# Performance work log

Measured on AMD Instinct MI355X. Metric: run time of the kernel, lower is better.

Reference implementation:

```python
import jax, jax.numpy as jnp
import numpy as np

N1, C, T1, V = 16, 64, 512, 25
NH, DK, DV, BD = 8, 64, 64, 64
DKH, DVH = DK // NH, DV // NH
NB = T1 // BD


def rel_to_abs(x):
    # x: (..., L, 2L-1) -> (..., L, L)  (rel-shift trick)
    *lead, L, _ = x.shape
    x = jnp.pad(x, [(0, 0)] * (x.ndim - 1) + [(0, 1)])      # (..., L, 2L)
    x = x.reshape(*lead, L * 2 * L)
    x = jnp.pad(x, [(0, 0)] * (x.ndim - 1) + [(0, L - 1)])
    x = x.reshape(*lead, L + 1, 2 * L - 1)
    return x[..., :L, L - 1:]


def setup_inputs() -> dict:
    key = jax.random.key(0)
    ks = jax.random.split(key, 6)
    return {
        "x": jax.random.normal(ks[0], (N1, C, T1, V), jnp.float32),
        "w_qkv": jax.random.normal(ks[1], (2 * DK + DV, C), jnp.float32) * 0.05,
        "b_qkv": jax.random.normal(ks[2], (2 * DK + DV,), jnp.float32) * 0.01,
        "w_out": jax.random.normal(ks[3], (DV, DV), jnp.float32) * 0.05,
        "b_out": jax.random.normal(ks[4], (DV,), jnp.float32) * 0.01,
        "key_rel": jax.random.normal(ks[5], (2 * BD - 1, DKH), jnp.float32),
    }


def reference(x, w_qkv, b_qkv, w_out, b_out, key_rel):
    B = N1 * V
    # (N1,C,T1,V) -> (N1*V, C, T1); 1x1 qkv conv == GEMM over channels
    xr = x.transpose(0, 3, 1, 2).reshape(B, C, T1)
    qkv = jnp.einsum('oc,bct->bot', w_qkv, xr) + b_qkv[None, :, None]
    q, k, v = qkv[:, :DK], qkv[:, DK:2 * DK], qkv[:, 2 * DK:]
    # split heads and blocks: (B, NH, dh, NB, BD); all blocks vectorized
    q = q.reshape(B, NH, DKH, NB, BD) * (DKH ** -0.5)
    k = k.reshape(B, NH, DKH, NB, BD)
    v = v.reshape(B, NH, DVH, NB, BD)
    logits = jnp.einsum('bhdnt,bhdns->bhnts', q, k)          # (B,NH,NB,BD,BD)
    # relative position logits (rel-shift)
    qb = q.transpose(0, 1, 3, 4, 2)                          # (B,NH,NB,BD,DKH)
    rel = jnp.einsum('bhntd,md->bhntm', qb, key_rel)         # (B,NH,NB,BD,2BD-1)
    logits = logits + rel_to_abs(rel)
    weights = jax.nn.softmax(logits, axis=-1)
    out = jnp.einsum('bhnts,bhdns->bhdnt', weights, v)       # (B,NH,DVH,NB,BD)
    # combine heads (head-major channels) and blocks along T
    out = out.reshape(B, DV, T1)
    ao = jnp.einsum('oc,bct->bot', w_out, out) + b_out[None, :, None]
    ao = ao.reshape(N1, V, DV, T1).transpose(0, 2, 3, 1)     # (N1,DV,T1,V)
    return jax.nn.relu(ao + x)
```

## Files before the change

kernel.cpp:

```cpp
#include <hip/hip_runtime.h>
#include <math.h>

#define Vc 25
#define QSCALE 0.5100697243f

#if __has_builtin(__builtin_amdgcn_mfma_f32_16x16x16bf16_1k)
#define HAVE_MFMA16 1
#define MFMA16(a, b, c) __builtin_amdgcn_mfma_f32_16x16x16bf16_1k(a, b, c, 0, 0, 0)
#else
#define HAVE_MFMA16 0
#endif

typedef short bf16x8 __attribute__((ext_vector_type(8), may_alias));
typedef short bf16x4 __attribute__((ext_vector_type(4), may_alias));
typedef unsigned int u32x2a __attribute__((ext_vector_type(2), may_alias));
typedef float f32x4 __attribute__((ext_vector_type(4)));

#define FENCE() asm volatile("" ::: "memory")

__device__ __forceinline__ unsigned short f2bf(float f) {
    unsigned u = __builtin_bit_cast(unsigned, f);
    u = (u + 0x7fff + ((u >> 16) & 1)) >> 16;
    return (unsigned short)u;
}
__device__ __forceinline__ unsigned short f2bf_fast(float f) {
    unsigned u = __builtin_bit_cast(unsigned, f) + 0x8000u;
    return (unsigned short)(u >> 16);
}
__device__ __forceinline__ unsigned pkbf(float lo, float hi) {
    unsigned a = __builtin_bit_cast(unsigned, lo) + 0x8000u;
    unsigned b = __builtin_bit_cast(unsigned, hi) + 0x8000u;
    return __builtin_amdgcn_perm(b, a, 0x07060302);
}
__device__ __forceinline__ float bf2f(unsigned short h) {
    unsigned u = ((unsigned)h) << 16;
    return __builtin_bit_cast(float, u);
}

template<int CTRL>
__device__ __forceinline__ float dpp_add(float x) {
    int xi = __builtin_bit_cast(int, x);
    int yi = __builtin_amdgcn_update_dpp(0, xi, CTRL, 0xf, 0xf, true);
    return x + __builtin_bit_cast(float, yi);
}
__device__ __forceinline__ float row_sum16(float s) {
    s = dpp_add<0xB1>(s);
    s = dpp_add<0x4E>(s);
    s = dpp_add<0x141>(s);
    s = dpp_add<0x140>(s);
    return s;
}

#define WQA_O 0
#define BQ_O  12288
#define KRT_O 12672
#define WOA_O 13760

__global__ void prep_kernel(const float* __restrict__ w_qkv, const float* __restrict__ b_qkv,
                            const float* __restrict__ w_out, const float* __restrict__ key_rel,
                            unsigned short* __restrict__ ws)
{
    const int gid = blockIdx.x * 256 + threadIdx.x;
    const int gsz = gridDim.x * 256;
    for (int id = gid; id < 12288; id += gsz) {
        int j = id & 7, lane = (id >> 3) & 63, ks = (id >> 9) & 1, mt = id >> 10;
        int m = mt * 16 + (lane & 15);
        int k = ks * 32 + (lane >> 4) * 8 + j;
        ws[WQA_O + id] = f2bf(w_qkv[m * 64 + k] * (m < 64 ? QSCALE : 1.f));
    }
    float* bq = (float*)(ws + BQ_O);
    for (int id = gid; id < 192; id += gsz)
        bq[id] = b_qkv[id] * (id < 64 ? QSCALE : 1.f);
    for (int id = gid; id < 1088; id += gsz) {
        int d = id & 7, m = id >> 3;
        ws[KRT_O + id] = (m < 127) ? f2bf(key_rel[m * 8 + d]) : (unsigned short)0;
    }
    for (int id = gid; id < 4096; id += gsz) {
        int j = id & 7, lane = (id >> 3) & 63, mtg = id >> 9;
        int m = (mtg & 3) * 16 + (lane & 15);
        int k = (mtg >> 2) * 32 + (lane >> 4) * 8 + j;
        ws[WOA_O + id] = f2bf(w_out[m * 64 + k]);
    }
}

#define QT_O   0
#define KT_O   4096
#define VS_O   8192
#define OT_O   12800
#define SCR_O  15360
#define SMEM_U16 19968

__global__ __launch_bounds__(256, 4)
void tcn_attn(const float* __restrict__ x, const float* __restrict__ b_out,
              const unsigned short* __restrict__ ws, float* __restrict__ y)
{
    __shared__ unsigned short sm[SMEM_U16];

    const int tid  = threadIdx.x;
    const int lane = tid & 63;
    const int w    = tid >> 6;
    const int li   = lane & 15;
    const int lq   = lane >> 4;
    const int koff = lq * 8;
    const int koff4 = lq * 4;
    const int n    = blockIdx.x;
    const int b    = blockIdx.y;
    const int n1   = b / Vc;
    const int v    = b - n1 * Vc;
    const int t0   = n * 64;
    const int trow = 16 * w + li;
    const unsigned scr = SCR_O + w * 1152;

    const bf16x8 z8 = {0,0,0,0,0,0,0,0};
    const bf16x4 z4h = {0,0,0,0};
    const f32x4  z4 = {0.f,0.f,0.f,0.f};
    (void)z4h; (void)koff4;

    for (int i = tid; i < 1920; i += 256)
        *(bf16x8*)(sm + i * 8) = z8;

    float xres[16];
    f32x4 pacc[4];
    #pragma unroll
    for (int mt = 0; mt < 4; ++mt)
        #pragma unroll
        for (int r = 0; r < 4; ++r) {
            int o = mt * 16 + lq * 4 + r;
            xres[mt * 4 + r] = x[((n1 * 64 + o) * 512 + t0 + 16 * w + li) * Vc + v];
            pacc[mt][r] = b_out[o];
        }

    #pragma unroll
    for (int mt = 0; mt < 4; ++mt)
        #pragma unroll
        for (int r = 0; r < 4; ++r)
            sm[SCR_O + (16 * w + li) * 72 + mt * 16 + 4 * lq + r] = f2bf_fast(xres[mt * 4 + r]);
    __syncthreads();

    const unsigned short* wq = ws + WQA_O;
    const float* bq = (const float*)(ws + BQ_O);
    #pragma unroll
    for (int sec = 0; sec < 3; ++sec) {
        const int mt = sec * 4 + w;
        bf16x8 a0 = *(const bf16x8*)(wq + ((mt * 2 + 0) * 64 + lane) * 8);
        bf16x8 a1 = *(const bf16x8*)(wq + ((mt * 2 + 1) * 64 + lane) * 8);
        f32x4 acc[4];
        __builtin_amdgcn_s_setprio(1);
        #pragma unroll
        for (int nt = 0; nt < 4; ++nt) {
            #pragma unroll
            for (int r = 0; r < 4; ++r) acc[nt][r] = bq[mt * 16 + lq * 4 + r];
            bf16x8 b0 = *(const bf16x8*)(sm + SCR_O + (16 * nt + li) * 72 + koff);
            bf16x8 b1 = *(const bf16x8*)(sm + SCR_O + (16 * nt + li) * 72 + 32 + koff);
            acc[nt] = __builtin_amdgcn_mfma_f32_16x16x32_bf16(a0, b0, acc[nt], 0, 0, 0);
            acc[nt] = __builtin_amdgcn_mfma_f32_16x16x32_bf16(a1, b1, acc[nt], 0, 0, 0);
        }
        __builtin_amdgcn_s_setprio(0);
        const int h2 = 2 * w + (lq >> 1);
        if (sec < 2) {
            const unsigned base = (sec == 0 ? QT_O : KT_O) + h2 * 512 + (lq & 1) * 4;
            #pragma unroll
            for (int nt = 0; nt < 4; ++nt) {
                u32x2a p;
                p.x = pkbf(acc[nt][0], acc[nt][1]);
                p.y = pkbf(acc[nt][2], acc[nt][3]);
                *(u32x2a*)(sm + base + (16 * nt + li) * 8) = p;
            }
        } else {
            #pragma unroll
            for (int nt = 0; nt < 4; ++nt)
                #pragma unroll
                for (int r = 0; r < 4; ++r)
                    sm[VS_O + h2 * 576 + ((lq & 1) * 4 + r) * 72 + 16 * nt + li] = f2bf_fast(acc[nt][r]);
        }
    }
    __syncthreads();

    int bidx[4];
    bool ghi[4];
    #pragma unroll
    for (int r = 0; r < 4; ++r) {
        int d = li - 4 * lq - r + 15;
        bidx[r] = ((lane & 48) | (d & 15)) << 2;
        ghi[r]  = d >= 16;
    }

#if HAVE_MFMA16
    bf16x4 br4[5];
    #pragma unroll
    for (int j = 0; j < 5; ++j)
        br4[j] = *(const bf16x4*)(ws + KRT_O + (16 * (3 - w + j) + li) * 8 + koff4);

    auto FRONT = [&](int h, f32x4* qk, f32x4* rl) {
        bf16x4 aq = *(const bf16x4*)(sm + QT_O + h * 512 + trow * 8 + koff4);
        if (lane >= 32) aq = z4h;
        __builtin_amdgcn_s_setprio(1);
        #pragma unroll
        for (int nt = 0; nt < 4; ++nt) {
            bf16x4 bk = *(const bf16x4*)(sm + KT_O + h * 512 + (16 * nt + li) * 8 + koff4);
            qk[nt] = MFMA16(aq, bk, z4);
        }
        #pragma unroll
        for (int j = 0; j < 5; ++j)
            rl[j] = MFMA16(aq, br4[j], z4);
        __builtin_amdgcn_s_setprio(0);
    };
#else
    bf16x8 br[5];
    #pragma unroll
    for (int j = 0; j < 5; ++j)
        br[j] = *(const bf16x8*)(ws + KRT_O + (16 * (3 - w + j) + li) * 8 + koff);

    auto FRONT = [&](int h, f32x4* qk, f32x4* rl) {
        bf16x8 aq = *(const bf16x8*)(sm + QT_O + h * 512 + trow * 8 + koff);
        if (lane >= 16) aq = z8;
        __builtin_amdgcn_s_setprio(1);
        #pragma unroll
        for (int nt = 0; nt < 4; ++nt) {
            bf16x8 bk = *(const bf16x8*)(sm + KT_O + h * 512 + (16 * nt + li) * 8 + koff);
            qk[nt] = __builtin_amdgcn_mfma_f32_16x16x32_bf16(aq, bk, z4, 0, 0, 0);
        }
        #pragma unroll
        for (int j = 0; j < 5; ++j)
            rl[j] = __builtin_amdgcn_mfma_f32_16x16x32_bf16(aq, br[j], z4, 0, 0, 0);
        __builtin_amdgcn_s_setprio(0);
    };
#endif

    auto BPERM = [&](const f32x4* rl, float (*sr)[5]) {
        #pragma unroll
        for (int r = 0; r < 4; ++r)
            #pragma unroll
            for (int j = 0; j < 5; ++j)
                sr[r][j] = __builtin_bit_cast(float,
                        __builtin_amdgcn_ds_bpermute(bidx[r], __builtin_bit_cast(int, rl[j][r])));
    };

    f32x4 qk[4];
    float sr[4][5];
    {
        f32x4 rl0[5];
        FRONT(0, qk, rl0);
        BPERM(rl0, sr);
    }

    #pragma unroll
    for (int h = 0; h < 8; ++h) {
        f32x4 qkn[4], rln[5];
        if (h < 7) FRONT(h + 1, qkn, rln);
        bf16x8 ao[4];
        if ((h & 3) == 3) {
            const int g = h >> 2;
            #pragma unroll
            for (int mt = 0; mt < 4; ++mt)
                ao[mt] = *(const bf16x8*)(ws + WOA_O + ((g * 4 + mt) * 64 + lane) * 8);
        }
        float lsum[4] = {0.f, 0.f, 0.f, 0.f};
        #pragma unroll
        for (int r = 0; r < 4; ++r)
            #pragma unroll
            for (int nt = 0; nt < 4; ++nt) {
                float rv = ghi[r] ? sr[r][nt + 1] : sr[r][nt];
                float e = __builtin_amdgcn_exp2f(qk[nt][r] + rv);
                sm[scr + (4 * lq + r) * 72 + 16 * nt + li] = f2bf_fast(e);
                lsum[r] += e;
            }
        float linv[4];
        #pragma unroll
        for (int r = 0; r < 4; ++r)
            linv[r] = 1.0f / row_sum16(lsum[r]);
        FENCE();
        f32x4 av = z4;
        __builtin_amdgcn_s_setprio(1);
        #pragma unroll
        for (int ks = 0; ks < 2; ++ks) {
            bf16x8 aa = *(const bf16x8*)(sm + scr + li * 72 + ks * 32 + koff);
            bf16x8 bv = *(const bf16x8*)(sm + VS_O + h * 576 + (li & 7) * 72 + ks * 32 + koff);
            av = __builtin_amdgcn_mfma_f32_16x16x32_bf16(aa, bv, av, 0, 0, 0);
        }
        __builtin_amdgcn_s_setprio(0);
        float srn[4][5];
        if (h < 7) BPERM(rln, srn);
        if (li < 8) {
            #pragma unroll
            for (int r = 0; r < 4; ++r)
                sm[OT_O + (16 * w + 4 * lq + r) * 40 + (h & 3) * 8 + li] = f2bf_fast(av[r] * linv[r]);
        }
        if ((h & 3) == 3) {
            FENCE();
            bf16x8 bo = *(const bf16x8*)(sm + OT_O + trow * 40 + koff);
            __builtin_amdgcn_s_setprio(1);
            #pragma unroll
            for (int mt = 0; mt < 4; ++mt)
                pacc[mt] = __builtin_amdgcn_mfma_f32_16x16x32_bf16(ao[mt], bo, pacc[mt], 0, 0, 0);
            __builtin_amdgcn_s_setprio(0);
        }
        FENCE();
        if (h < 7) {
            #pragma unroll
            for (int i = 0; i < 4; ++i) qk[i] = qkn[i];
            #pragma unroll
            for (int r = 0; r < 4; ++r)
                #pragma unroll
                for (int j = 0; j < 5; ++j)
                    sr[r][j] = srn[r][j];
        }
    }

    #pragma unroll
    for (int mt = 0; mt < 4; ++mt)
        #pragma unroll
        for (int r = 0; r < 4; ++r) {
            int o = mt * 16 + lq * 4 + r;
            int idx = ((n1 * 64 + o) * 512 + t0 + 16 * w + li) * Vc + v;
            y[idx] = fmaxf(pacc[mt][r] + xres[mt * 4 + r], 0.f);
        }
}

extern "C" void kernel_launch(void* const* d_in, const int* in_sizes, int n_in,
                              void* d_out, int out_size, void* d_ws, size_t ws_size,
                              hipStream_t stream) {
    const float* x       = (const float*)d_in[0];
    const float* w_qkv   = (const float*)d_in[1];
    const float* b_qkv   = (const float*)d_in[2];
    const float* w_out   = (const float*)d_in[3];
    const float* b_out   = (const float*)d_in[4];
    const float* key_rel = (const float*)d_in[5];
    float* y = (float*)d_out;
    unsigned short* ws = (unsigned short*)d_ws;

    prep_kernel<<<dim3(96), dim3(256), 0, stream>>>(w_qkv, b_qkv, w_out, key_rel, ws);
    dim3 grid(512 / 64, 400);
    tcn_attn<<<grid, dim3(256), 0, stream>>>(x, b_out, ws, y);
}
```

Baseline: 203.5 us.

## Process two adjacent V columns per block with paired 8-byte global loads/stores

Each block now handles two neighbouring v indices (the last group handles one). x is read and y written as float2 pairs, and the whole attention pipeline runs twice per block. The aim is to halve the strided 4-byte global transactions over the innermost V dimension, which waste sector bandwidth, and to halve the grid size. In exchange each block does serial work for two columns, register pressure rises from holding two residual arrays, and the block count drops to 1664.

```diff
diff --git a/kernel.cpp b/kernel.cpp
--- a/kernel.cpp
+++ b/kernel.cpp
@@ -15,6 +15,7 @@
 typedef short bf16x4 __attribute__((ext_vector_type(4), may_alias));
 typedef unsigned int u32x2a __attribute__((ext_vector_type(2), may_alias));
 typedef float f32x4 __attribute__((ext_vector_type(4)));
+typedef float f32x2a __attribute__((ext_vector_type(2), aligned(4), may_alias));
 
 #define FENCE() asm volatile("" ::: "memory")
 
@@ -105,8 +106,10 @@
     const int koff4 = lq * 4;
     const int n    = blockIdx.x;
     const int b    = blockIdx.y;
-    const int n1   = b / Vc;
-    const int v    = b - n1 * Vc;
+    const int n1   = b / 13;
+    const int vg   = b - n1 * 13;
+    const int v0   = vg * 2;
+    const int nv   = (vg < 12) ? 2 : 1;
     const int t0   = n * 64;
     const int trow = 16 * w + li;
     const unsigned scr = SCR_O + w * 1152;
@@ -119,62 +122,27 @@
     for (int i = tid; i < 1920; i += 256)
         *(bf16x8*)(sm + i * 8) = z8;
 
-    float xres[16];
-    f32x4 pacc[4];
-    #pragma unroll
-    for (int mt = 0; mt < 4; ++mt)
-        #pragma unroll
-        for (int r = 0; r < 4; ++r) {
-            int o = mt * 16 + lq * 4 + r;
-            xres[mt * 4 + r] = x[((n1 * 64 + o) * 512 + t0 + 16 * w + li) * Vc + v];
-            pacc[mt][r] = b_out[o];
-        }
-
-    #pragma unroll
-    for (int mt = 0; mt < 4; ++mt)
-        #pragma unroll
-        for (int r = 0; r < 4; ++r)
-            sm[SCR_O + (16 * w + li) * 72 + mt * 16 + 4 * lq + r] = f2bf_fast(xres[mt * 4 + r]);
-    __syncthreads();
-
-    const unsigned short* wq = ws + WQA_O;
-    const float* bq = (const float*)(ws + BQ_O);
-    #pragma unroll
-    for (int sec = 0; sec < 3; ++sec) {
-        const int mt = sec * 4 + w;
-        bf16x8 a0 = *(const bf16x8*)(wq + ((mt * 2 + 0) * 64 + lane) * 8);
-        bf16x8 a1 = *(const bf16x8*)(wq + ((mt * 2 + 1) * 64 + lane) * 8);
-        f32x4 acc[4];
-        __builtin_amdgcn_s_setprio(1);
-        #pragma unroll
-        for (int nt = 0; nt < 4; ++nt) {
-            #pragma unroll
-            for (int r = 0; r < 4; ++r) acc[nt][r] = bq[mt * 16 + lq * 4 + r];
-            bf16x8 b0 = *(const bf16x8*)(sm + SCR_O + (16 * nt + li) * 72 + koff);
-            bf16x8 b1 = *(const bf16x8*)(sm + SCR_O + (16 * nt + li) * 72 + 32 + koff);
-            acc[nt] = __builtin_amdgcn_mfma_f32_16x16x32_bf16(a0, b0, acc[nt], 0, 0, 0);
-            acc[nt] = __builtin_amdgcn_mfma_f32_16x16x32_bf16(a1, b1, acc[nt], 0, 0, 0);
-        }
-        __builtin_amdgcn_s_setprio(0);
-        const int h2 = 2 * w + (lq >> 1);
-        if (sec < 2) {
-            const unsigned base = (sec == 0 ? QT_O : KT_O) + h2 * 512 + (lq & 1) * 4;
-            #pragma unroll
-            for (int nt = 0; nt < 4; ++nt) {
-                u32x2a p;
-                p.x = pkbf(acc[nt][0], acc[nt][1]);
-                p.y = pkbf(acc[nt][2], acc[nt][3]);
-                *(u32x2a*)(sm + base + (16 * nt + li) * 8) = p;
-            }
-        } else {
-            #pragma unroll
-            for (int nt = 0; nt < 4; ++nt)
-                #pragma unroll
-                for (int r = 0; r < 4; ++r)
-                    sm[VS_O + h2 * 576 + ((lq & 1) * 4 + r) * 72 + 16 * nt + li] = f2bf_fast(acc[nt][r]);
-        }
-    }
-    __syncthreads();
+    float xr0[16], xr1[16];
+    if (nv == 2) {
+        #pragma unroll
+        for (int mt = 0; mt < 4; ++mt)
+            #pragma unroll
+            for (int r = 0; r < 4; ++r) {
+                int o = mt * 16 + lq * 4 + r;
+                f32x2a p = *(const f32x2a*)&x[((n1 * 64 + o) * 512 + t0 + trow) * Vc + v0];
+                xr0[mt * 4 + r] = p.x;
+                xr1[mt * 4 + r] = p.y;
+            }
+    } else {
+        #pragma unroll
+        for (int mt = 0; mt < 4; ++mt)
+            #pragma unroll
+            for (int r = 0; r < 4; ++r) {
+                int o = mt * 16 + lq * 4 + r;
+                xr0[mt * 4 + r] = x[((n1 * 64 + o) * 512 + t0 + trow) * Vc + v0];
+                xr1[mt * 4 + r] = 0.f;
+            }
+    }
 
     int bidx[4];
     bool ghi[4];
@@ -184,6 +152,9 @@
         bidx[r] = ((lane & 48) | (d & 15)) << 2;
         ghi[r]  = d >= 16;
     }
+
+    const unsigned short* wq = ws + WQA_O;
+    const float* bq = (const float*)(ws + BQ_O);
 
 #if HAVE_MFMA16
     bf16x4 br4[5];
@@ -236,85 +207,157 @@
                         __builtin_amdgcn_ds_bpermute(bidx[r], __builtin_bit_cast(int, rl[j][r])));
     };
 
-    f32x4 qk[4];
-    float sr[4][5];
-    {
-        f32x4 rl0[5];
-        FRONT(0, qk, rl0);
-        BPERM(rl0, sr);
-    }
-
-    #pragma unroll
-    for (int h = 0; h < 8; ++h) {
-        f32x4 qkn[4], rln[5];
-        if (h < 7) FRONT(h + 1, qkn, rln);
-        bf16x8 ao[4];
-        if ((h & 3) == 3) {
-            const int g = h >> 2;
-            #pragma unroll
-            for (int mt = 0; mt < 4; ++mt)
-                ao[mt] = *(const bf16x8*)(ws + WOA_O + ((g * 4 + mt) * 64 + lane) * 8);
-        }
-        float lsum[4] = {0.f, 0.f, 0.f, 0.f};
-        #pragma unroll
-        for (int r = 0; r < 4; ++r)
+    auto DOV = [&](const float (&xr)[16], float (&yout)[16]) {
+        #pragma unroll
+        for (int mt = 0; mt < 4; ++mt)
+            #pragma unroll
+            for (int r = 0; r < 4; ++r)
+                sm[SCR_O + trow * 72 + mt * 16 + 4 * lq + r] = f2bf_fast(xr[mt * 4 + r]);
+        __syncthreads();
+
+        #pragma unroll
+        for (int sec = 0; sec < 3; ++sec) {
+            const int mt = sec * 4 + w;
+            bf16x8 a0 = *(const bf16x8*)(wq + ((mt * 2 + 0) * 64 + lane) * 8);
+            bf16x8 a1 = *(const bf16x8*)(wq + ((mt * 2 + 1) * 64 + lane) * 8);
+            f32x4 acc[4];
+            __builtin_amdgcn_s_setprio(1);
             #pragma unroll
             for (int nt = 0; nt < 4; ++nt) {
-                float rv = ghi[r] ? sr[r][nt + 1] : sr[r][nt];
-                float e = __builtin_amdgcn_exp2f(qk[nt][r] + rv);
-                sm[scr + (4 * lq + r) * 72 + 16 * nt + li] = f2bf_fast(e);
-                lsum[r] += e;
-            }
-        float linv[4];
-        #pragma unroll
-        for (int r = 0; r < 4; ++r)
-            linv[r] = 1.0f / row_sum16(lsum[r]);
-        FENCE();
-        f32x4 av = z4;
-        __builtin_amdgcn_s_setprio(1);
-        #pragma unroll
-        for (int ks = 0; ks < 2; ++ks) {
-            bf16x8 aa = *(const bf16x8*)(sm + scr + li * 72 + ks * 32 + koff);
-            bf16x8 bv = *(const bf16x8*)(sm + VS_O + h * 576 + (li & 7) * 72 + ks * 32 + koff);
-            av = __builtin_amdgcn_mfma_f32_16x16x32_bf16(aa, bv, av, 0, 0, 0);
-        }
-        __builtin_amdgcn_s_setprio(0);
-        float srn[4][5];
-        if (h < 7) BPERM(rln, srn);
-        if (li < 8) {
-            #pragma unroll
-            for (int r = 0; r < 4; ++r)
-                sm[OT_O + (16 * w + 4 * lq + r) * 40 + (h & 3) * 8 + li] = f2bf_fast(av[r] * linv[r]);
-        }
-        if ((h & 3) == 3) {
+                #pragma unroll
+                for (int r = 0; r < 4; ++r) acc[nt][r] = bq[mt * 16 + lq * 4 + r];
+                bf16x8 b0 = *(const bf16x8*)(sm + SCR_O + (16 * nt + li) * 72 + koff);
+                bf16x8 b1 = *(const bf16x8*)(sm + SCR_O + (16 * nt + li) * 72 + 32 + koff);
+                acc[nt] = __builtin_amdgcn_mfma_f32_16x16x32_bf16(a0, b0, acc[nt], 0, 0, 0);
+                acc[nt] = __builtin_amdgcn_mfma_f32_16x16x32_bf16(a1, b1, acc[nt], 0, 0, 0);
+            }
+            __builtin_amdgcn_s_setprio(0);
+            const int h2 = 2 * w + (lq >> 1);
+            if (sec < 2) {
+                const unsigned base = (sec == 0 ? QT_O : KT_O) + h2 * 512 + (lq & 1) * 4;
+                #pragma unroll
+                for (int nt = 0; nt < 4; ++nt) {
+                    u32x2a p;
+                    p.x = pkbf(acc[nt][0], acc[nt][1]);
+                    p.y = pkbf(acc[nt][2], acc[nt][3]);
+                    *(u32x2a*)(sm + base + (16 * nt + li) * 8) = p;
+                }
+            } else {
+                #pragma unroll
+                for (int nt = 0; nt < 4; ++nt)
+                    #pragma unroll
+                    for (int r = 0; r < 4; ++r)
+                        sm[VS_O + h2 * 576 + ((lq & 1) * 4 + r) * 72 + 16 * nt + li] = f2bf_fast(acc[nt][r]);
+            }
+        }
+        __syncthreads();
+
+        f32x4 pacc[4];
+        #pragma unroll
+        for (int mt = 0; mt < 4; ++mt)
+            #pragma unroll
+            for (int r = 0; r < 4; ++r)
+                pacc[mt][r] = b_out[mt * 16 + lq * 4 + r];
+
+        f32x4 qk[4];
+        float sr[4][5];
+        {
+            f32x4 rl0[5];
+            FRONT(0, qk, rl0);
+            BPERM(rl0, sr);
+        }
+
+        #pragma unroll
+        for (int h = 0; h < 8; ++h) {
+            f32x4 qkn[4], rln[5];
+            if (h < 7) FRONT(h + 1, qkn, rln);
+            bf16x8 ao[4];
+            if ((h & 3) == 3) {
+                const int g = h >> 2;
+                #pragma unroll
+                for (int mt = 0; mt < 4; ++mt)
+                    ao[mt] = *(const bf16x8*)(ws + WOA_O + ((g * 4 + mt) * 64 + lane) * 8);
+            }
+            float lsum[4] = {0.f, 0.f, 0.f, 0.f};
+            #pragma unroll
+            for (int r = 0; r < 4; ++r)
+                #pragma unroll
+                for (int nt = 0; nt < 4; ++nt) {
+                    float rv = ghi[r] ? sr[r][nt + 1] : sr[r][nt];
+                    float e = __builtin_amdgcn_exp2f(qk[nt][r] + rv);
+                    sm[scr + (4 * lq + r) * 72 + 16 * nt + li] = f2bf_fast(e);
+                    lsum[r] += e;
+                }
+            float linv[4];
+            #pragma unroll
+            for (int r = 0; r < 4; ++r)
+                linv[r] = 1.0f / row_sum16(lsum[r]);
             FENCE();
-            bf16x8 bo = *(const bf16x8*)(sm + OT_O + trow * 40 + koff);
+            f32x4 av = z4;
             __builtin_amdgcn_s_setprio(1);
             #pragma unroll
-            for (int mt = 0; mt < 4; ++mt)
-                pacc[mt] = __builtin_amdgcn_mfma_f32_16x16x32_bf16(ao[mt], bo, pacc[mt], 0, 0, 0);
+            for (int ks = 0; ks < 2; ++ks) {
+                bf16x8 aa = *(const bf16x8*)(sm + scr + li * 72 + ks * 32 + koff);
+                bf16x8 bv = *(const bf16x8*)(sm + VS_O + h * 576 + (li & 7) * 72 + ks * 32 + koff);
+                av = __builtin_amdgcn_mfma_f32_16x16x32_bf16(aa, bv, av, 0, 0, 0);
+            }
             __builtin_amdgcn_s_setprio(0);
-        }
-        FENCE();
-        if (h < 7) {
-            #pragma unroll
-            for (int i = 0; i < 4; ++i) qk[i] = qkn[i];
-            #pragma unroll
-            for (int r = 0; r < 4; ++r)
-                #pragma unroll
-                for (int j = 0; j < 5; ++j)
-                    sr[r][j] = srn[r][j];
-        }
-    }
-
-    #pragma unroll
-    for (int mt = 0; mt < 4; ++mt)
-        #pragma unroll
-        for (int r = 0; r < 4; ++r) {
-            int o = mt * 16 + lq * 4 + r;
-            int idx = ((n1 * 64 + o) * 512 + t0 + 16 * w + li) * Vc + v;
-            y[idx] = fmaxf(pacc[mt][r] + xres[mt * 4 + r], 0.f);
-        }
+            float srn[4][5];
+            if (h < 7) BPERM(rln, srn);
+            if (li < 8) {
+                #pragma unroll
+                for (int r = 0; r < 4; ++r)
+                    sm[OT_O + (16 * w + 4 * lq + r) * 40 + (h & 3) * 8 + li] = f2bf_fast(av[r] * linv[r]);
+            }
+            if ((h & 3) == 3) {
+                FENCE();
+                bf16x8 bo = *(const bf16x8*)(sm + OT_O + trow * 40 + koff);
+                __builtin_amdgcn_s_setprio(1);
+                #pragma unroll
+                for (int mt = 0; mt < 4; ++mt)
+                    pacc[mt] = __builtin_amdgcn_mfma_f32_16x16x32_bf16(ao[mt], bo, pacc[mt], 0, 0, 0);
+                __builtin_amdgcn_s_setprio(0);
+            }
+            FENCE();
+            if (h < 7) {
+                #pragma unroll
+                for (int i = 0; i < 4; ++i) qk[i] = qkn[i];
+                #pragma unroll
+                for (int r = 0; r < 4; ++r)
+                    #pragma unroll
+                    for (int j = 0; j < 5; ++j)
+                        sr[r][j] = srn[r][j];
+            }
+        }
+
+        #pragma unroll
+        for (int mt = 0; mt < 4; ++mt)
+            #pragma unroll
+            for (int r = 0; r < 4; ++r)
+                yout[mt * 4 + r] = fmaxf(pacc[mt][r] + xr[mt * 4 + r], 0.f);
+    };
+
+    float y0[16], y1[16];
+    DOV(xr0, y0);
+    if (nv == 2) {
+        DOV(xr1, y1);
+        #pragma unroll
+        for (int mt = 0; mt < 4; ++mt)
+            #pragma unroll
+            for (int r = 0; r < 4; ++r) {
+                int o = mt * 16 + lq * 4 + r;
+                f32x2a p; p.x = y0[mt * 4 + r]; p.y = y1[mt * 4 + r];
+                *(f32x2a*)&y[((n1 * 64 + o) * 512 + t0 + trow) * Vc + v0] = p;
+            }
+    } else {
+        #pragma unroll
+        for (int mt = 0; mt < 4; ++mt)
+            #pragma unroll
+            for (int r = 0; r < 4; ++r) {
+                int o = mt * 16 + lq * 4 + r;
+                y[((n1 * 64 + o) * 512 + t0 + trow) * Vc + v0] = y0[mt * 4 + r];
+            }
+    }
 }
 
 extern "C" void kernel_launch(void* const* d_in, const int* in_sizes, int n_in,
@@ -330,6 +373,6 @@
     unsigned short* ws = (unsigned short*)d_ws;
 
     prep_kernel<<<dim3(96), dim3(256), 0, stream>>>(w_qkv, b_qkv, w_out, key_rel, ws);
-    dim3 grid(512 / 64, 400);
+    dim3 grid(8, 208);
     tcn_attn<<<grid, dim3(256), 0, stream>>>(x, b_out, ws, y);
 }
```

After: 247.7 us. 21.7% more time.
